# Optimization experiments

Hardware: AMD Instinct MI355X
Metric: run time of the kernel (lower is better)

The kernel has to match this reference:

```python
import jax, jax.numpy as jnp
import numpy as np

B, H, E, V = 128, 1024, 1024, 40000
L, S, A = 256, 10, 10
L_S, L_A = 1.0, 1.0  # s_copy_lambda / a_copy_lambda
NEG = -1e24


def setup_inputs():
    key = jax.random.key(0)
    ks = jax.random.split(key, 32)
    n = lambda i, shape: jax.random.normal(ks[i], shape, dtype=jnp.float32)
    p = lambda i, shape: jax.random.normal(ks[i], shape, dtype=jnp.float32) * 0.02
    rnn_in = 3 * E + H  # embed + history ctx (H) + state ctx (E) + action ctx (E)
    return {
        "inp": n(0, (B, 1, E)),
        "hidden": n(1, (1, B, H)),
        "hs_vectors": n(2, (B, L, H)),
        "state_gumbel_prob": jax.random.uniform(ks[3], (B, S, V), dtype=jnp.float32),
        "state_gumbel_embed": n(4, (B, S, E)),
        "action_gumbel_prob": jax.random.uniform(ks[5], (B, A, V), dtype=jnp.float32),
        "action_gumbel_embed": n(6, (B, A, E)),
        "history_lens": jax.random.randint(ks[7], (B,), 1, L + 1),
        "history_word_indices": jax.random.randint(ks[8], (B, L), 0, V),
        # history word mlp-attention
        "Wq_hist": p(9, (H, H)), "bq_hist": jnp.zeros((H,), jnp.float32),
        "Wm_hist": p(10, (H, H)), "v_hist": p(11, (H,)),
        # init_s_attn / init_a_attn (query H, memory E)
        "Wq_s": p(12, (H, H)), "bq_s": jnp.zeros((H,), jnp.float32),
        "Wm_s": p(13, (E, H)), "v_s": p(14, (H,)),
        "Wq_a": p(15, (H, H)), "bq_a": jnp.zeros((H,), jnp.float32),
        "Wm_a": p(16, (E, H)), "v_a": p(17, (H,)),
        # sparse_copy_attn (memory E+1)
        "Wq_sc": p(18, (H, H)), "bq_sc": jnp.zeros((H,), jnp.float32),
        "Wm_sc": p(19, (E + 1, H)), "v_sc": p(20, (H,)),
        # GRU (torch layout: [3H, in], gate order r,z,n)
        "W_ih": p(21, (3 * H, rnn_in)), "W_hh": p(22, (3 * H, H)),
        "b_ih": jnp.zeros((3 * H,), jnp.float32), "b_hh": jnp.zeros((3 * H,), jnp.float32),
        # output projection
        "W_out": p(23, (H, V)), "b_out": jnp.zeros((V,), jnp.float32),
    }


def _mlp_scores(q, mem, Wq, bq, Wm, v):
    # q: [B,1,H], mem: [B,L,M] -> additive-attention logits [B,1,L]
    t = jnp.tanh((q @ Wq + bq) + (mem @ Wm))  # [B,L,H]
    return (t @ v)[:, None, :]


def reference(inp, hidden, hs_vectors, state_gumbel_prob, state_gumbel_embed,
              action_gumbel_prob, action_gumbel_embed, history_lens,
              history_word_indices, Wq_hist, bq_hist, Wm_hist, v_hist,
              Wq_s, bq_s, Wm_s, v_s, Wq_a, bq_a, Wm_a, v_a,
              Wq_sc, bq_sc, Wm_sc, v_sc, W_ih, W_hh, b_ih, b_hh, W_out, b_out):
    q0 = jnp.transpose(hidden, (1, 0, 2))  # [B,1,H]
    # --- history word attention (masked mlp attention) ---
    hist_scores = _mlp_scores(q0, hs_vectors, Wq_hist, bq_hist, Wm_hist, v_hist)
    valid = jnp.arange(L)[None, None, :] < history_lens[:, None, None]
    hist_scores = jnp.where(valid, hist_scores, NEG)
    c_his = jax.nn.softmax(hist_scores, axis=-1) @ hs_vectors  # [B,1,H]
    # --- init_consult over state / action gumbel embeddings ---
    sw = jax.nn.softmax(_mlp_scores(q0, state_gumbel_embed, Wq_s, bq_s, Wm_s, v_s), axis=-1)
    c_state = sw @ state_gumbel_embed  # [B,1,E]
    aw = jax.nn.softmax(_mlp_scores(q0, action_gumbel_embed, Wq_a, bq_a, Wm_a, v_a), axis=-1)
    c_action = aw @ action_gumbel_embed  # [B,1,E]
    x = jnp.concatenate([inp, c_his, c_state, c_action], axis=-1)[:, 0, :]  # [B,3E+H]
    # --- single-step GRU cell (torch semantics, gate order r,z,n) ---
    h0 = hidden[0]
    gi = x @ W_ih.T + b_ih
    gh = h0 @ W_hh.T + b_hh
    ir, iz, inn = jnp.split(gi, 3, axis=-1)
    hr, hz, hn = jnp.split(gh, 3, axis=-1)
    r = jax.nn.sigmoid(ir + hr)
    z = jax.nn.sigmoid(iz + hz)
    nact = jnp.tanh(inn + r * hn)
    h_new = (1.0 - z) * nact + z * h0  # [B,H]
    # --- vocab logits + copy logits, joint softmax ---
    gene_logits = h_new @ W_out + b_out  # [B,V]
    cq = h_new[:, None, :]
    hs_logits = jnp.einsum('bqh,blh->bql', cq, hs_vectors)[:, 0, :]  # dot attn, [B,L]
    s_tag = jnp.zeros((B, S, 1), jnp.float32)
    a_tag = jnp.ones((B, A, 1), jnp.float32)
    st_logits = _mlp_scores(cq, jnp.concatenate([state_gumbel_embed, s_tag], -1), Wq_sc, bq_sc, Wm_sc, v_sc)[:, 0, :]
    ac_logits = _mlp_scores(cq, jnp.concatenate([action_gumbel_embed, a_tag], -1), Wq_sc, bq_sc, Wm_sc, v_sc)[:, 0, :]
    all_logits = jnp.concatenate([gene_logits, hs_logits, st_logits, ac_logits], axis=-1)
    wp = jax.nn.softmax(all_logits, axis=-1)  # [B, V+L+S+A]
    gene_p = wp[:, :V]
    hs_w = wp[:, V:V + L]
    st_w = wp[:, V + L:V + L + S]
    ac_w = wp[:, V + L + S:]
    # --- copy-distribution mixing ---
    scp = jnp.einsum('bs,bsv->bv', st_w, state_gumbel_prob)
    acp = jnp.einsum('ba,bav->bv', ac_w, action_gumbel_prob)
    gene_p = gene_p + L_S * scp + L_A * acp
    copy_p = jnp.zeros((B, V), jnp.float32).at[jnp.arange(B)[:, None], history_word_indices].add(hs_w)
    out = jnp.log(gene_p + copy_p)[:, None, :]  # [B,1,V]
    return out, h_new[None]
```

## Files before the change

### kernel.cpp

```cpp
#include <hip/hip_runtime.h>
#include <stdint.h>

typedef __attribute__((ext_vector_type(4))) float f32x4;
typedef __attribute__((ext_vector_type(2))) unsigned int u32x2;
typedef __attribute__((ext_vector_type(4))) unsigned int u32x4;
typedef __attribute__((ext_vector_type(8))) short bf16x8;

#define BV (128*40000)

__device__ __forceinline__ unsigned rne_bf16(float f) {
    unsigned x = __float_as_uint(f);
    return ((x + 0x7FFFu + ((x >> 16) & 1u)) >> 16) & 0xFFFFu;
}
__device__ __forceinline__ unsigned pack2(float a, float b) {
    return rne_bf16(a) | (rne_bf16(b) << 16);
}
__device__ __forceinline__ float bf2f(unsigned u) {
    return __uint_as_float((u & 0xFFFFu) << 16);
}
__device__ __forceinline__ float sigm(float x) { return 1.0f / (1.0f + expf(-x)); }
__device__ __forceinline__ float ftanh(float x) {
    float e = __expf(2.0f * x);
    return 1.0f - 2.0f / (e + 1.0f);
}

__device__ __forceinline__ void gload16(const void* g, void* l) {
    __builtin_amdgcn_global_load_lds(
        (const __attribute__((address_space(1))) unsigned*)g,
        (__attribute__((address_space(3))) unsigned*)l, 16, 0, 0);
}

struct BigArgs {
    const unsigned short *hs, *WmhT, *se, *ae, *WmsT, *WmaT;
    const int* lens;
    const float *qh_h, *bq_h, *v_h;
    const float *qh_s, *bq_s, *v_s;
    const float *qh_a, *bq_a, *v_a;
    float *hsc, *stsc, *acsc;
};

__global__ __launch_bounds__(512, 1) void k_big(BigArgs a) {
    __shared__ unsigned short As[2][16384];
    __shared__ unsigned short Bs[2][16384];

    int bid = blockIdx.x;
    int wg = (bid & 7) * 69 + (bid >> 3);

    const unsigned short *A, *Bt;
    const float *rb, *cb, *vv;
    float* out;
    int m0, n0, vrows, rpb;
    if (wg < 512) {
        int m = wg >> 2, n = wg & 3;
        A = a.hs; Bt = a.WmhT; rb = a.qh_h; cb = a.bq_h; vv = a.v_h; out = a.hsc;
        m0 = m << 8; n0 = n << 8; vrows = a.lens[m]; rpb = 256;
    } else {
        int r = wg - 512;
        int op = r / 20; r -= op * 20;
        int mt = r >> 2, nt = r & 3;
        if (op == 0) { A = a.se; Bt = a.WmsT; rb = a.qh_s; cb = a.bq_s; vv = a.v_s; out = a.stsc; }
        else         { A = a.ae; Bt = a.WmaT; rb = a.qh_a; cb = a.bq_a; vv = a.v_a; out = a.acsc; }
        m0 = mt << 8; n0 = nt << 8; vrows = 256; rpb = 10;
    }

    const int t = threadIdx.x, lane = t & 63, wv = t >> 6;
    const int l16 = lane & 15, lq = lane >> 4;
    const int wm = wv >> 2, wn = wv & 3;

    const int srowL = t >> 3;
    const int gccA = ((t & 7) ^ (srowL & 7)) << 3;
    const unsigned short* gA = A + (size_t)(m0 + srowL) * 1024 + gccA;
    const unsigned short* gB = Bt + (size_t)(n0 + srowL) * 1024 + gccA;

    f32x4 acc[8][4];
#pragma unroll
    for (int i = 0; i < 8; ++i)
#pragma unroll
        for (int j = 0; j < 4; ++j) acc[i][j] = (f32x4){0.f, 0.f, 0.f, 0.f};

    const int sw = l16 & 7;
    const int c0 = ((lq ^ sw) << 3);
    const int A0 = (wm << 13) + (l16 << 6);
    const int B0 = ((wn >> 1) << 13) + ((((wn & 1) << 6) + l16) << 6);

#define STAGE(kt, d)                                                          \
    {                                                                         \
        const unsigned short* ga_ = gA + (size_t)(kt) * 64;                   \
        const unsigned short* gb_ = gB + (size_t)(kt) * 64;                   \
        _Pragma("unroll")                                                     \
        for (int h_ = 0; h_ < 2; ++h_) {                                      \
            _Pragma("unroll")                                                 \
            for (int r_ = 0; r_ < 2; ++r_) {                                  \
                size_t go_ = (size_t)(h_ * 128 + r_ * 64) * 1024;             \
                int lo_ = h_ * 8192 + r_ * 4096 + (wv << 9);                  \
                gload16(ga_ + go_, &As[d][lo_]);                              \
                gload16(gb_ + go_, &Bs[d][lo_]);                              \
            }                                                                 \
        }                                                                     \
    }

    STAGE(0, 0);
    for (int kt = 0; kt < 16; ++kt) {
        int cur = kt & 1;
        if (kt < 15) {
            STAGE(kt + 1, cur ^ 1);
            asm volatile("s_waitcnt vmcnt(8)" ::: "memory");
        } else {
            asm volatile("s_waitcnt vmcnt(0)" ::: "memory");
        }
        __builtin_amdgcn_s_barrier();
        __builtin_amdgcn_sched_barrier(0);

        const unsigned short* ab = As[cur];
        const unsigned short* bb = Bs[cur];
        if (vrows > (wm << 7)) {
            bf16x8 bf[4][2];
#pragma unroll
            for (int nf = 0; nf < 4; ++nf) {
                bf[nf][0] = *(const bf16x8*)(bb + B0 + (nf << 10) + c0);
                bf[nf][1] = *(const bf16x8*)(bb + B0 + (nf << 10) + (c0 ^ 32));
            }
#pragma unroll
            for (int mf = 0; mf < 8; ++mf) {
                if ((wm << 7) + (mf << 4) < vrows) {
                    bf16x8 a0 = *(const bf16x8*)(ab + A0 + (mf << 10) + c0);
                    bf16x8 a1 = *(const bf16x8*)(ab + A0 + (mf << 10) + (c0 ^ 32));
#pragma unroll
                    for (int nf = 0; nf < 4; ++nf) {
                        acc[mf][nf] = __builtin_amdgcn_mfma_f32_16x16x32_bf16(a0, bf[nf][0], acc[mf][nf], 0, 0, 0);
                        acc[mf][nf] = __builtin_amdgcn_mfma_f32_16x16x32_bf16(a1, bf[nf][1], acc[mf][nf], 0, 0, 0);
                    }
                }
            }
        }
        __builtin_amdgcn_sched_barrier(0);
        __builtin_amdgcn_s_barrier();
    }
#undef STAGE

    float cbv[4], vvv[4];
    int gcs[4];
#pragma unroll
    for (int nf = 0; nf < 4; ++nf) {
        int gc = n0 + (wn << 6) + (nf << 4) + l16;
        gcs[nf] = gc; cbv[nf] = cb[gc]; vvv[nf] = vv[gc];
    }
#pragma unroll
    for (int mf = 0; mf < 8; ++mf) {
        int rloc = (wm << 7) + (mf << 4);
        if (rloc < vrows) {
#pragma unroll
            for (int r = 0; r < 4; ++r) {
                int gr = m0 + rloc + (lq << 2) + r;
                const float* rbp = rb + (size_t)(gr / rpb) * 1024;
                float s = 0.f;
#pragma unroll
                for (int nf = 0; nf < 4; ++nf) {
                    float x = acc[mf][nf][r] + rbp[gcs[nf]] + cbv[nf];
                    s += ftanh(x) * vvv[nf];
                }
#pragma unroll
                for (int m2 = 1; m2 < 16; m2 <<= 1) s += __shfl_xor(s, m2, 64);
                if (l16 == 0) atomicAdd(&out[gr], s);
            }
        }
    }
}

template<int EPI>
__device__ __forceinline__ void mgemm(
    const unsigned short* __restrict__ A, const unsigned short* __restrict__ Bt,
    float* __restrict__ out, const float* __restrict__ rb,
    const float* __restrict__ cb1, const float* __restrict__ cb2,
    const float* __restrict__ vvec,
    int m0, int n0, int kb, int ke, int ldk, int ldc, int rpb)
{
    __shared__ unsigned short As[2][4096];
    __shared__ unsigned short Bs[2][4096];
    const int t = threadIdx.x, lane = t & 63, wv = t >> 6;
    const int l16 = lane & 15, lq = lane >> 4;
    const int wm = wv >> 1, wn = wv & 1;

    const int srow = lane >> 2, scol = (lane & 3) << 3;
    const unsigned short* gA0 = A + (size_t)(m0 + (wv << 4) + srow) * ldk + kb + scol;
    const unsigned short* gA1 = gA0 + (size_t)64 * ldk;
    const unsigned short* gB0 = Bt + (size_t)(n0 + (wv << 4) + srow) * ldk + kb + scol;
    const unsigned short* gB1 = gB0 + (size_t)64 * ldk;
    unsigned short* lA0 = &As[0][wv << 9];
    unsigned short* lA1 = &As[0][(wv + 4) << 9];
    unsigned short* lB0 = &Bs[0][wv << 9];
    unsigned short* lB1 = &Bs[0][(wv + 4) << 9];

    f32x4 acc[4][4];
#pragma unroll
    for (int i = 0; i < 4; ++i)
#pragma unroll
        for (int j = 0; j < 4; ++j) acc[i][j] = (f32x4){0.f, 0.f, 0.f, 0.f};

    const int NS = (ke - kb) >> 5;
    gload16(gA0, lA0); gload16(gA1, lA1);
    gload16(gB0, lB0); gload16(gB1, lB1);

    for (int s = 0; s < NS; ++s) {
        __syncthreads();
        if (s + 1 < NS) {
            const int nb = (s + 1) & 1, ko = (s + 1) << 5;
            gload16(gA0 + ko, lA0 + (nb << 12)); gload16(gA1 + ko, lA1 + (nb << 12));
            gload16(gB0 + ko, lB0 + (nb << 12)); gload16(gB1 + ko, lB1 + (nb << 12));
        }
        const unsigned short* ab = As[s & 1];
        const unsigned short* bb = Bs[s & 1];
        bf16x8 af[4], bfv[4];
#pragma unroll
        for (int i = 0; i < 4; ++i)
            af[i] = *(const bf16x8*)(ab + (((wm << 6) + (i << 4) + l16) << 5) + (lq << 3));
#pragma unroll
        for (int i = 0; i < 4; ++i)
            bfv[i] = *(const bf16x8*)(bb + (((wn << 6) + (i << 4) + l16) << 5) + (lq << 3));
#pragma unroll
        for (int mf = 0; mf < 4; ++mf)
#pragma unroll
            for (int nf = 0; nf < 4; ++nf)
                acc[mf][nf] = __builtin_amdgcn_mfma_f32_16x16x32_bf16(af[mf], bfv[nf], acc[mf][nf], 0, 0, 0);
    }

    if (EPI == 1) {
#pragma unroll
        for (int mf = 0; mf < 4; ++mf) {
#pragma unroll
            for (int r = 0; r < 4; ++r) {
                int gr = m0 + (wm << 6) + (mf << 4) + (lq << 2) + r;
                const float* rbp = rb + (size_t)(gr / rpb) * 1024;
                float s = 0.0f;
#pragma unroll
                for (int nf = 0; nf < 4; ++nf) {
                    int gc = n0 + (wn << 6) + (nf << 4) + l16;
                    float xv = acc[mf][nf][r] + rbp[gc] + cb1[gc];
                    if (cb2) xv += cb2[gc];
                    s += ftanh(xv) * vvec[gc];
                }
#pragma unroll
                for (int msk = 1; msk < 16; msk <<= 1) s += __shfl_xor(s, msk, 64);
                if (l16 == 0) atomicAdd(&out[gr], s);
            }
        }
    } else {
#pragma unroll
        for (int mf = 0; mf < 4; ++mf) {
            int gr0 = m0 + (wm << 6) + (mf << 4) + (lq << 2);
#pragma unroll
            for (int nf = 0; nf < 4; ++nf) {
                int gc = n0 + (wn << 6) + (nf << 4) + l16;
#pragma unroll
                for (int r = 0; r < 4; ++r)
                    atomicAdd(&out[(size_t)(gr0 + r) * ldc + gc], acc[mf][nf][r]);
            }
        }
    }
}

__device__ __forceinline__ void gene_body(
    const unsigned short* __restrict__ hnb, const float* __restrict__ Wout,
    const float* __restrict__ b_out, float* __restrict__ out, int n0)
{
    __shared__ unsigned short As[2][4096];
    __shared__ unsigned short Bs[2][4096];
    const int t = threadIdx.x, lane = t & 63, wv = t >> 6;
    const int l16 = lane & 15, lq = lane >> 4;
    const int wm = wv >> 1, wn = wv & 1;

    const int srow = lane >> 2, scol = (lane & 3) << 3;
    const unsigned short* gA0 = hnb + (size_t)((wv << 4) + srow) * 1024 + scol;
    const unsigned short* gA1 = gA0 + (size_t)64 * 1024;
    unsigned short* lA0 = &As[0][wv << 9];
    unsigned short* lA1 = &As[0][(wv + 4) << 9];

    const int bn = t & 127, kh = t >> 7;
    const bool ok = (n0 + bn) < 40000;
    const float* gB = Wout + (size_t)(kh * 16) * 40000 + (n0 + bn);

    f32x4 acc[4][4];
#pragma unroll
    for (int i = 0; i < 4; ++i)
#pragma unroll
        for (int j = 0; j < 4; ++j) acc[i][j] = (f32x4){0.f, 0.f, 0.f, 0.f};

    auto stageB = [&](int buf, int ko) {
        const float* src = gB + (size_t)ko * 40000;
        float f[16];
#pragma unroll
        for (int j = 0; j < 16; ++j) f[j] = ok ? src[(size_t)j * 40000] : 0.0f;
        u32x4* d = (u32x4*)&Bs[buf][bn * 32 + kh * 16];
        d[0] = (u32x4){pack2(f[0],f[1]), pack2(f[2],f[3]), pack2(f[4],f[5]), pack2(f[6],f[7])};
        d[1] = (u32x4){pack2(f[8],f[9]), pack2(f[10],f[11]), pack2(f[12],f[13]), pack2(f[14],f[15])};
    };

    gload16(gA0, lA0); gload16(gA1, lA1); stageB(0, 0);
    for (int s = 0; s < 32; ++s) {
        __syncthreads();
        if (s + 1 < 32) {
            const int nb = (s + 1) & 1, ko = (s + 1) << 5;
            gload16(gA0 + ko, lA0 + (nb << 12)); gload16(gA1 + ko, lA1 + (nb << 12));
            stageB(nb, ko);
        }
        const unsigned short* ab = As[s & 1];
        const unsigned short* bb = Bs[s & 1];
        bf16x8 af[4], bfv[4];
#pragma unroll
        for (int i = 0; i < 4; ++i)
            af[i] = *(const bf16x8*)(ab + (((wm << 6) + (i << 4) + l16) << 5) + (lq << 3));
#pragma unroll
        for (int i = 0; i < 4; ++i)
            bfv[i] = *(const bf16x8*)(bb + (((wn << 6) + (i << 4) + l16) << 5) + (lq << 3));
#pragma unroll
        for (int mf = 0; mf < 4; ++mf)
#pragma unroll
            for (int nf = 0; nf < 4; ++nf)
                acc[mf][nf] = __builtin_amdgcn_mfma_f32_16x16x32_bf16(af[mf], bfv[nf], acc[mf][nf], 0, 0, 0);
    }
#pragma unroll
    for (int mf = 0; mf < 4; ++mf) {
        int gr0 = (wm << 6) + (mf << 4) + (lq << 2);
#pragma unroll
        for (int nf = 0; nf < 4; ++nf) {
            int gc = n0 + (wn << 6) + (nf << 4) + l16;
            if (gc < 40000) {
                float bo = b_out[gc];
#pragma unroll
                for (int r = 0; r < 4; ++r)
                    out[(size_t)(gr0 + r) * 40000 + gc] = acc[mf][nf][r] + bo;
            }
        }
    }
}

__global__ __launch_bounds__(256) void k_stac3(
    const unsigned short* se, const unsigned short* ae, const unsigned short* WmscT,
    const float* tagrow, const float* qsc, const float* bq_sc, const float* v_sc,
    float* stlg, float* aclg) {
    if (blockIdx.z == 0)
        mgemm<1>(se, WmscT, stlg, qsc, bq_sc, nullptr, v_sc, blockIdx.y * 128, blockIdx.x * 128, 0, 1024, 1024, 0, 10);
    else
        mgemm<1>(ae, WmscT, aclg, qsc, bq_sc, tagrow, v_sc, blockIdx.y * 128, blockIdx.x * 128, 0, 1024, 1024, 0, 10);
}

__global__ __launch_bounds__(256) void k_qh4(
    const unsigned short* q0, const unsigned short* W0, const unsigned short* W1,
    const unsigned short* W2, float* o0, float* o1, float* o2) {
    const unsigned short* W = W0; float* o = o0;
    if (blockIdx.z == 1) { W = W1; o = o1; }
    if (blockIdx.z == 2) { W = W2; o = o2; }
    int kb = blockIdx.y << 8;
    mgemm<2>(q0, W, o, nullptr, nullptr, nullptr, nullptr, 0, blockIdx.x * 128, kb, kb + 256, 1024, 1024, 1);
}

__global__ __launch_bounds__(256) void k_gigh2(
    const unsigned short* xb, const unsigned short* q0,
    const unsigned short* Wih, const unsigned short* Whh, float* gi, float* gh) {
    if (blockIdx.z == 0) {
        int kb = blockIdx.y << 9;
        mgemm<2>(xb, Wih, gi, nullptr, nullptr, nullptr, nullptr, 0, blockIdx.x * 128, kb, kb + 512, 4096, 3072, 1);
    } else {
        if (blockIdx.y >= 2) return;
        int kb = blockIdx.y << 9;
        mgemm<2>(q0, Whh, gh, nullptr, nullptr, nullptr, nullptr, 0, blockIdx.x * 128, kb, kb + 512, 1024, 3072, 1);
    }
}

__global__ __launch_bounds__(256) void k_qsc_gene(
    const unsigned short* hnb, const unsigned short* WqscT, float* qsc,
    const float* Wout, const float* b_out, float* out) {
    int id = blockIdx.x;
    if (id < 16) {
        int x = id & 7, kb = (id >> 3) << 9;
        mgemm<2>(hnb, WqscT, qsc, nullptr, nullptr, nullptr, nullptr, 0, x * 128, kb, kb + 512, 1024, 1024, 1);
    } else {
        gene_body(hnb, Wout, b_out, out, (id - 16) << 7);
    }
}

struct CvtArgs { const float* s[6]; unsigned short* d[6]; int pre[7]; };
__global__ __launch_bounds__(256) void k_cvt_all(CvtArgs a) {
    int total = a.pre[6];
    for (int i = blockIdx.x * 256 + threadIdx.x; i < total; i += gridDim.x * 256) {
        int seg = 0;
        while (i >= a.pre[seg + 1]) ++seg;
        int loc = i - a.pre[seg];
        const f32x4* s4 = (const f32x4*)a.s[seg] + (size_t)loc * 2;
        f32x4 q0 = s4[0], q1 = s4[1];
        ((u32x4*)a.d[seg])[loc] =
            (u32x4){pack2(q0[0],q0[1]), pack2(q0[2],q0[3]), pack2(q1[0],q1[1]), pack2(q1[2],q1[3])};
    }
}

struct TrArgs { const float* s[8]; unsigned short* d[8]; };
__global__ __launch_bounds__(256) void k_trcvt(TrArgs a) {
    __shared__ float tile[64][65];
    const float* in = a.s[blockIdx.z];
    unsigned short* ot = a.d[blockIdx.z];
    int k0 = blockIdx.y << 6, n0 = blockIdx.x << 6;
    int tr = threadIdx.x >> 6, tc = threadIdx.x & 63;
#pragma unroll
    for (int i = 0; i < 16; ++i) {
        int r = (i << 2) + tr;
        tile[r][tc] = in[(size_t)(k0 + r) * 1024 + n0 + tc];
    }
    __syncthreads();
#pragma unroll
    for (int i = 0; i < 16; ++i) {
        int r = (i << 2) + tr;
        ot[(size_t)(n0 + r) * 1024 + k0 + tc] = (unsigned short)rne_bf16(tile[tc][r]);
    }
}

__device__ __forceinline__ void softmax10(const float* src, float* dst) {
    float m = src[0];
    for (int i = 1; i < 10; ++i) m = fmaxf(m, src[i]);
    float z = 0.f, e[10];
    for (int i = 0; i < 10; ++i) { e[i] = expf(src[i] - m); z += e[i]; }
    float iz = 1.0f / z;
    for (int i = 0; i < 10; ++i) dst[i] = e[i] * iz;
}

__global__ __launch_bounds__(256) void k_ctx(
    const float* __restrict__ scores, const int* __restrict__ lens,
    const unsigned short* __restrict__ hs,
    const float* __restrict__ inp, const float* __restrict__ st_sc, const float* __restrict__ ac_sc,
    const unsigned short* __restrict__ se, const unsigned short* __restrict__ ae,
    unsigned short* __restrict__ xb) {
    int b = blockIdx.x, t = threadIdx.x;
    __shared__ float w[256];
    __shared__ float red[256];
    __shared__ float sw[10], aw[10];
    int len = lens[b];
    float s = scores[b * 256 + t];
    bool valid = t < len;
    red[t] = valid ? s : -3.0e38f;
    __syncthreads();
    for (int st = 128; st > 0; st >>= 1) { if (t < st) red[t] = fmaxf(red[t], red[t + st]); __syncthreads(); }
    float m = red[0];
    __syncthreads();
    float e = valid ? expf(s - m) : 0.0f;
    red[t] = e;
    __syncthreads();
    for (int st = 128; st > 0; st >>= 1) { if (t < st) red[t] += red[t + st]; __syncthreads(); }
    float Z = red[0];
    __syncthreads();
    w[t] = e / Z;
    if (t == 0) softmax10(st_sc + b * 10, sw);
    if (t == 64) softmax10(ac_sc + b * 10, aw);
    f32x4 iv = ((const f32x4*)(inp + (size_t)b * 1024))[t];
    *((u32x2*)(xb + (size_t)b * 4096) + t) = (u32x2){pack2(iv[0], iv[1]), pack2(iv[2], iv[3])};
    __syncthreads();
    float a0 = 0.f, a1 = 0.f, a2 = 0.f, a3 = 0.f;
    for (int l = 0; l < 256; ++l) {
        float wl = w[l];
        if (wl == 0.0f) continue;
        u32x2 u = *((const u32x2*)(hs + ((size_t)b * 256 + l) * 1024) + t);
        a0 += wl * bf2f(u[0]); a1 += wl * bf2f(u[0] >> 16);
        a2 += wl * bf2f(u[1]); a3 += wl * bf2f(u[1] >> 16);
    }
    *((u32x2*)(xb + (size_t)b * 4096 + 1024) + t) = (u32x2){pack2(a0, a1), pack2(a2, a3)};
    float cs0=0,cs1=0,cs2=0,cs3=0, ca0=0,ca1=0,ca2=0,ca3=0;
#pragma unroll
    for (int q = 0; q < 10; ++q) {
        u32x2 us = *((const u32x2*)(se + ((size_t)b * 10 + q) * 1024) + t);
        u32x2 ua = *((const u32x2*)(ae + ((size_t)b * 10 + q) * 1024) + t);
        float ws = sw[q], wa = aw[q];
        cs0 += ws * bf2f(us[0]); cs1 += ws * bf2f(us[0] >> 16);
        cs2 += ws * bf2f(us[1]); cs3 += ws * bf2f(us[1] >> 16);
        ca0 += wa * bf2f(ua[0]); ca1 += wa * bf2f(ua[0] >> 16);
        ca2 += wa * bf2f(ua[1]); ca3 += wa * bf2f(ua[1] >> 16);
    }
    *((u32x2*)(xb + (size_t)b * 4096 + 2048) + t) = (u32x2){pack2(cs0, cs1), pack2(cs2, cs3)};
    *((u32x2*)(xb + (size_t)b * 4096 + 3072) + t) = (u32x2){pack2(ca0, ca1), pack2(ca2, ca3)};
}

__global__ __launch_bounds__(1024) void k_gruhsl(
    const float* __restrict__ gi, const float* __restrict__ gh,
    const float* __restrict__ b_ih, const float* __restrict__ b_hh,
    const float* __restrict__ h0, float* __restrict__ hnew,
    unsigned short* __restrict__ hnb,
    const unsigned short* __restrict__ hs, float* __restrict__ hsl) {
    int b = blockIdx.x, j = threadIdx.x;
    size_t i = (size_t)b * 1024 + j;
    const float* gib = gi + (size_t)b * 3072;
    const float* ghb = gh + (size_t)b * 3072;
    float r = sigm(gib[j] + b_ih[j] + ghb[j] + b_hh[j]);
    float z = sigm(gib[1024 + j] + b_ih[1024 + j] + ghb[1024 + j] + b_hh[1024 + j]);
    float hn = ghb[2048 + j] + b_hh[2048 + j];
    float n = tanhf(gib[2048 + j] + b_ih[2048 + j] + r * hn);
    float h = (1.0f - z) * n + z * h0[i];
    hnew[i] = h;
    hnb[i] = (unsigned short)rne_bf16(h);
    __shared__ float hsm[1024];
    hsm[j] = h;
    __syncthreads();
    int wave = j >> 6, lane = j & 63;
    float hr[16];
#pragma unroll
    for (int k = 0; k < 16; ++k) hr[k] = hsm[lane * 16 + k];
    for (int l = wave; l < 256; l += 16) {
        const u32x4* row = (const u32x4*)(hs + ((size_t)b * 256 + l) * 1024);
        u32x4 u0 = row[lane * 2], u1 = row[lane * 2 + 1];
        float s = hr[0]*bf2f(u0[0]) + hr[1]*bf2f(u0[0]>>16) + hr[2]*bf2f(u0[1]) + hr[3]*bf2f(u0[1]>>16)
                + hr[4]*bf2f(u0[2]) + hr[5]*bf2f(u0[2]>>16) + hr[6]*bf2f(u0[3]) + hr[7]*bf2f(u0[3]>>16)
                + hr[8]*bf2f(u1[0]) + hr[9]*bf2f(u1[0]>>16) + hr[10]*bf2f(u1[1]) + hr[11]*bf2f(u1[1]>>16)
                + hr[12]*bf2f(u1[2]) + hr[13]*bf2f(u1[2]>>16) + hr[14]*bf2f(u1[3]) + hr[15]*bf2f(u1[3]>>16);
#pragma unroll
        for (int msk = 1; msk < 64; msk <<= 1) s += __shfl_xor(s, msk, 64);
        if (lane == 0) hsl[b * 256 + l] = s;
    }
}

__global__ __launch_bounds__(256) void k_smsc(
    const float* __restrict__ gene, const float* __restrict__ hsl,
    const float* __restrict__ stl, const float* __restrict__ acl,
    const int* __restrict__ hwi,
    float* __restrict__ mbuf, float* __restrict__ zbuf, float* __restrict__ copyp) {
    int b = blockIdx.x, t = threadIdx.x;
    __shared__ float red[256];
    const f32x4* g4 = (const f32x4*)(gene + (size_t)b * 40000);
    float mx = -3.0e38f;
    for (int i = t; i < 10000; i += 256) {
        f32x4 q = g4[i];
        mx = fmaxf(mx, fmaxf(fmaxf(q[0], q[1]), fmaxf(q[2], q[3])));
    }
    float hv = hsl[b * 256 + t];
    mx = fmaxf(mx, hv);
    if (t < 10) mx = fmaxf(mx, fmaxf(stl[b * 10 + t], acl[b * 10 + t]));
    red[t] = mx; __syncthreads();
    for (int s = 128; s > 0; s >>= 1) { if (t < s) red[t] = fmaxf(red[t], red[t + s]); __syncthreads(); }
    float m = red[0];
    __syncthreads();
    float sum = 0.f;
    for (int i = t; i < 10000; i += 256) {
        f32x4 q = g4[i];
        sum += expf(q[0]-m) + expf(q[1]-m) + expf(q[2]-m) + expf(q[3]-m);
    }
    sum += expf(hv - m);
    if (t < 10) sum += expf(stl[b * 10 + t] - m) + expf(acl[b * 10 + t] - m);
    red[t] = sum; __syncthreads();
    for (int s = 128; s > 0; s >>= 1) { if (t < s) red[t] += red[t + s]; __syncthreads(); }
    float Z = red[0];
    if (t == 0) { mbuf[b] = m; zbuf[b] = Z; }
    float wv = expf(hv - m) / Z;
    atomicAdd(copyp + (size_t)b * 40000 + hwi[b * 256 + t], wv);
}

__global__ __launch_bounds__(256) void k_final(
    float* __restrict__ gene_out, const float* __restrict__ copyp,
    const float* __restrict__ sprob, const float* __restrict__ aprob,
    const float* __restrict__ stl, const float* __restrict__ acl,
    const float* __restrict__ mbuf, const float* __restrict__ zbuf) {
    int b = blockIdx.y, t = threadIdx.x;
    __shared__ float sw[10], aw[10];
    float m = mbuf[b], iz = 1.0f / zbuf[b];
    if (t < 10) sw[t] = expf(stl[b * 10 + t] - m) * iz;
    if (t >= 64 && t < 74) aw[t - 64] = expf(acl[b * 10 + (t - 64)] - m) * iz;
    __syncthreads();
    int v4 = blockIdx.x * 256 + t;
    if (v4 < 10000) {
        size_t base = (size_t)b * 10000 + v4;
        f32x4 g = ((const f32x4*)gene_out)[base];
        f32x4 c = ((const f32x4*)copyp)[base];
        f32x4 acc;
#pragma unroll
        for (int j = 0; j < 4; ++j) acc[j] = expf(g[j] - m) * iz + c[j];
#pragma unroll
        for (int s = 0; s < 10; ++s) {
            f32x4 pv = ((const f32x4*)sprob)[((size_t)b * 10 + s) * 10000 + v4];
            f32x4 av = ((const f32x4*)aprob)[((size_t)b * 10 + s) * 10000 + v4];
            float ws = sw[s], wa = aw[s];
#pragma unroll
            for (int j = 0; j < 4; ++j) acc[j] += ws * pv[j] + wa * av[j];
        }
        f32x4 r;
#pragma unroll
        for (int j = 0; j < 4; ++j) r[j] = logf(acc[j]);
        ((f32x4*)gene_out)[base] = r;
    }
}

#define OFF_QH_H  0
#define OFF_QH_S  131072
#define OFF_QH_A  262144
#define OFF_QSC   393216
#define OFF_GI    524288
#define OFF_GH    917504
#define OFF_HSC   1310720
#define OFF_STSC  1343488
#define OFF_ACSC  1344768
#define OFF_STLG  1346048
#define OFF_ACLG  1347328
#define ZERO_FLOATS 1348608
#define OFF_HSL   1348608
#define OFF_M     1381376
#define OFF_Z     1381504
#define OFF_COPY  1381632
#define FLOAT_TOTAL 6501632
#define SO_HS     0
#define SO_SE     33554432
#define SO_AE     34865152
#define SO_Q0     36175872
#define SO_X      36306944
#define SO_HNB    36831232
#define SO_WQHT   36962304
#define SO_WQST   38010880
#define SO_WQAT   39059456
#define SO_WQSCT  40108032
#define SO_WMHT   41156608
#define SO_WMST   42205184
#define SO_WMAT   43253760
#define SO_WMSCT  44302336
#define SO_WIH    45350912
#define SO_WHH    57933824

extern "C" void kernel_launch(void* const* d_in, const int* in_sizes, int n_in,
                              void* d_out, int out_size, void* d_ws, size_t ws_size,
                              hipStream_t stream) {
    const float* inp     = (const float*)d_in[0];
    const float* hidden  = (const float*)d_in[1];
    const float* hs      = (const float*)d_in[2];
    const float* sprob   = (const float*)d_in[3];
    const float* se      = (const float*)d_in[4];
    const float* aprob   = (const float*)d_in[5];
    const float* ae      = (const float*)d_in[6];
    const int*   lens    = (const int*)d_in[7];
    const int*   hwi     = (const int*)d_in[8];
    const float* Wq_hist = (const float*)d_in[9];
    const float* bq_hist = (const float*)d_in[10];
    const float* Wm_hist = (const float*)d_in[11];
    const float* v_hist  = (const float*)d_in[12];
    const float* Wq_s    = (const float*)d_in[13];
    const float* bq_s    = (const float*)d_in[14];
    const float* Wm_s    = (const float*)d_in[15];
    const float* v_s     = (const float*)d_in[16];
    const float* Wq_a    = (const float*)d_in[17];
    const float* bq_a    = (const float*)d_in[18];
    const float* Wm_a    = (const float*)d_in[19];
    const float* v_a     = (const float*)d_in[20];
    const float* Wq_sc   = (const float*)d_in[21];
    const float* bq_sc   = (const float*)d_in[22];
    const float* Wm_sc   = (const float*)d_in[23];
    const float* v_sc    = (const float*)d_in[24];
    const float* W_ih    = (const float*)d_in[25];
    const float* W_hh    = (const float*)d_in[26];
    const float* b_ih    = (const float*)d_in[27];
    const float* b_hh    = (const float*)d_in[28];
    const float* W_out   = (const float*)d_in[29];
    const float* b_out   = (const float*)d_in[30];

    float* out  = (float*)d_out;
    float* w    = (float*)d_ws;
    float* hnew = out + BV;
    unsigned short* sb = (unsigned short*)(w + FLOAT_TOTAL);

    float* qh_h = w + OFF_QH_H;  float* qh_s = w + OFF_QH_S;  float* qh_a = w + OFF_QH_A;
    float* qsc  = w + OFF_QSC;   float* gi   = w + OFF_GI;    float* gh   = w + OFF_GH;
    float* hsc  = w + OFF_HSC;   float* stsc = w + OFF_STSC;  float* acsc = w + OFF_ACSC;
    float* stlg = w + OFF_STLG;  float* aclg = w + OFF_ACLG;
    float* hsl  = w + OFF_HSL;   float* mbuf = w + OFF_M;     float* zbuf = w + OFF_Z;
    float* copyp = w + OFF_COPY;

    unsigned short* hs_bf = sb + SO_HS;   unsigned short* se_bf = sb + SO_SE;
    unsigned short* ae_bf = sb + SO_AE;   unsigned short* q0_bf = sb + SO_Q0;
    unsigned short* x_bf  = sb + SO_X;    unsigned short* hnb   = sb + SO_HNB;
    unsigned short* WqhT  = sb + SO_WQHT; unsigned short* WqsT  = sb + SO_WQST;
    unsigned short* WqaT  = sb + SO_WQAT; unsigned short* WqscT = sb + SO_WQSCT;
    unsigned short* WmhT  = sb + SO_WMHT; unsigned short* WmsT  = sb + SO_WMST;
    unsigned short* WmaT  = sb + SO_WMAT; unsigned short* WmscT = sb + SO_WMSCT;
    unsigned short* WihB  = sb + SO_WIH;  unsigned short* WhhB  = sb + SO_WHH;

    dim3 blk(256);

    hipMemsetAsync(w, 0, (size_t)ZERO_FLOATS * 4, stream);
    hipMemsetAsync(copyp, 0, (size_t)BV * 4, stream);

    CvtArgs ca;
    ca.s[0]=hs; ca.s[1]=se; ca.s[2]=ae; ca.s[3]=hidden; ca.s[4]=W_ih; ca.s[5]=W_hh;
    ca.d[0]=hs_bf; ca.d[1]=se_bf; ca.d[2]=ae_bf; ca.d[3]=q0_bf; ca.d[4]=WihB; ca.d[5]=WhhB;
    ca.pre[0]=0; ca.pre[1]=4194304; ca.pre[2]=4358144; ca.pre[3]=4521984;
    ca.pre[4]=4538368; ca.pre[5]=6111232; ca.pre[6]=6504448;
    k_cvt_all<<<dim3(4096), blk, 0, stream>>>(ca);

    TrArgs ta;
    ta.s[0]=Wq_hist; ta.s[1]=Wq_s; ta.s[2]=Wq_a; ta.s[3]=Wq_sc;
    ta.s[4]=Wm_hist; ta.s[5]=Wm_s; ta.s[6]=Wm_a; ta.s[7]=Wm_sc;
    ta.d[0]=WqhT; ta.d[1]=WqsT; ta.d[2]=WqaT; ta.d[3]=WqscT;
    ta.d[4]=WmhT; ta.d[5]=WmsT; ta.d[6]=WmaT; ta.d[7]=WmscT;
    k_trcvt<<<dim3(16, 16, 8), blk, 0, stream>>>(ta);

    k_qh4<<<dim3(8, 4, 3), blk, 0, stream>>>(q0_bf, WqhT, WqsT, WqaT, qh_h, qh_s, qh_a);

    BigArgs ba;
    ba.hs = hs_bf; ba.WmhT = WmhT; ba.se = se_bf; ba.ae = ae_bf;
    ba.WmsT = WmsT; ba.WmaT = WmaT; ba.lens = lens;
    ba.qh_h = qh_h; ba.bq_h = bq_hist; ba.v_h = v_hist;
    ba.qh_s = qh_s; ba.bq_s = bq_s; ba.v_s = v_s;
    ba.qh_a = qh_a; ba.bq_a = bq_a; ba.v_a = v_a;
    ba.hsc = hsc; ba.stsc = stsc; ba.acsc = acsc;
    k_big<<<dim3(552), dim3(512), 0, stream>>>(ba);

    k_ctx<<<dim3(128), blk, 0, stream>>>(hsc, lens, hs_bf, inp, stsc, acsc, se_bf, ae_bf, x_bf);
    k_gigh2<<<dim3(24, 8, 2), blk, 0, stream>>>(x_bf, q0_bf, WihB, WhhB, gi, gh);
    k_gruhsl<<<dim3(128), dim3(1024), 0, stream>>>(gi, gh, b_ih, b_hh, hidden, hnew, hnb, hs_bf, hsl);
    k_qsc_gene<<<dim3(329), blk, 0, stream>>>(hnb, WqscT, qsc, W_out, b_out, out);
    k_stac3<<<dim3(8, 10, 2), blk, 0, stream>>>(se_bf, ae_bf, WmscT, Wm_sc + (size_t)1024 * 1024,
                                                qsc, bq_sc, v_sc, stlg, aclg);
    k_smsc<<<dim3(128), blk, 0, stream>>>(out, hsl, stlg, aclg, hwi, mbuf, zbuf, copyp);
    k_final<<<dim3(40, 128), blk, 0, stream>>>(out, copyp, sprob, aprob, stlg, aclg, mbuf, zbuf);

    (void)in_sizes; (void)n_in; (void)out_size; (void)ws_size;
}
```

Baseline: 575.4 us.

## Make k_big a persistent kernel with an atomic tile counter

Changes the big attention-score GEMM kernel from one workgroup per tile (552 blocks) to 256 persistent workgroups that take tiles from a global atomic counter. The small state/action tiles are scheduled first, followed by the history tiles, whose cost varies with history length. This targets the load imbalance caused by masked rows and the tail effect of a fixed grid. It adds a counter in the zeroed workspace, plus an atomic and two block barriers per tile. The MFMA issue order inside each k-step is also regrouped.

```diff
diff --git a/kernel.cpp b/kernel.cpp
--- a/kernel.cpp
+++ b/kernel.cpp
@@ -39,29 +39,10 @@
     float *hsc, *stsc, *acsc;
 };
 
-__global__ __launch_bounds__(512, 1) void k_big(BigArgs a) {
+__global__ __launch_bounds__(512, 1) void k_big(BigArgs a, int* __restrict__ ctr) {
     __shared__ unsigned short As[2][16384];
     __shared__ unsigned short Bs[2][16384];
-
-    int bid = blockIdx.x;
-    int wg = (bid & 7) * 69 + (bid >> 3);
-
-    const unsigned short *A, *Bt;
-    const float *rb, *cb, *vv;
-    float* out;
-    int m0, n0, vrows, rpb;
-    if (wg < 512) {
-        int m = wg >> 2, n = wg & 3;
-        A = a.hs; Bt = a.WmhT; rb = a.qh_h; cb = a.bq_h; vv = a.v_h; out = a.hsc;
-        m0 = m << 8; n0 = n << 8; vrows = a.lens[m]; rpb = 256;
-    } else {
-        int r = wg - 512;
-        int op = r / 20; r -= op * 20;
-        int mt = r >> 2, nt = r & 3;
-        if (op == 0) { A = a.se; Bt = a.WmsT; rb = a.qh_s; cb = a.bq_s; vv = a.v_s; out = a.stsc; }
-        else         { A = a.ae; Bt = a.WmaT; rb = a.qh_a; cb = a.bq_a; vv = a.v_a; out = a.acsc; }
-        m0 = mt << 8; n0 = nt << 8; vrows = 256; rpb = 10;
-    }
+    __shared__ int sTile;
 
     const int t = threadIdx.x, lane = t & 63, wv = t >> 6;
     const int l16 = lane & 15, lq = lane >> 4;
@@ -69,15 +50,6 @@
 
     const int srowL = t >> 3;
     const int gccA = ((t & 7) ^ (srowL & 7)) << 3;
-    const unsigned short* gA = A + (size_t)(m0 + srowL) * 1024 + gccA;
-    const unsigned short* gB = Bt + (size_t)(n0 + srowL) * 1024 + gccA;
-
-    f32x4 acc[8][4];
-#pragma unroll
-    for (int i = 0; i < 8; ++i)
-#pragma unroll
-        for (int j = 0; j < 4; ++j) acc[i][j] = (f32x4){0.f, 0.f, 0.f, 0.f};
-
     const int sw = l16 & 7;
     const int c0 = ((lq ^ sw) << 3);
     const int A0 = (wm << 13) + (l16 << 6);
@@ -99,72 +71,107 @@
         }                                                                     \
     }
 
-    STAGE(0, 0);
-    for (int kt = 0; kt < 16; ++kt) {
-        int cur = kt & 1;
-        if (kt < 15) {
-            STAGE(kt + 1, cur ^ 1);
-            asm volatile("s_waitcnt vmcnt(8)" ::: "memory");
+    for (;;) {
+        __syncthreads();
+        if (t == 0) sTile = atomicAdd(ctr, 1);
+        __syncthreads();
+        const int wg = sTile;
+        if (wg >= 552) return;
+
+        const unsigned short *A, *Bt;
+        const float *rb, *cb, *vv;
+        float* out;
+        int m0, n0, vrows, rpb;
+        if (wg < 40) {
+            int op = wg / 20, r = wg - op * 20;
+            int mt = r >> 2, nt = r & 3;
+            if (op == 0) { A = a.se; Bt = a.WmsT; rb = a.qh_s; cb = a.bq_s; vv = a.v_s; out = a.stsc; }
+            else         { A = a.ae; Bt = a.WmaT; rb = a.qh_a; cb = a.bq_a; vv = a.v_a; out = a.acsc; }
+            m0 = mt << 8; n0 = nt << 8; vrows = 256; rpb = 10;
         } else {
-            asm volatile("s_waitcnt vmcnt(0)" ::: "memory");
-        }
-        __builtin_amdgcn_s_barrier();
-        __builtin_amdgcn_sched_barrier(0);
-
-        const unsigned short* ab = As[cur];
-        const unsigned short* bb = Bs[cur];
-        if (vrows > (wm << 7)) {
-            bf16x8 bf[4][2];
-#pragma unroll
-            for (int nf = 0; nf < 4; ++nf) {
-                bf[nf][0] = *(const bf16x8*)(bb + B0 + (nf << 10) + c0);
-                bf[nf][1] = *(const bf16x8*)(bb + B0 + (nf << 10) + (c0 ^ 32));
+            int h = wg - 40;
+            int m = h >> 2, n = h & 3;
+            A = a.hs; Bt = a.WmhT; rb = a.qh_h; cb = a.bq_h; vv = a.v_h; out = a.hsc;
+            m0 = m << 8; n0 = n << 8; vrows = a.lens[m]; rpb = 256;
+        }
+
+        const unsigned short* gA = A + (size_t)(m0 + srowL) * 1024 + gccA;
+        const unsigned short* gB = Bt + (size_t)(n0 + srowL) * 1024 + gccA;
+
+        f32x4 acc[8][4];
+#pragma unroll
+        for (int i = 0; i < 8; ++i)
+#pragma unroll
+            for (int j = 0; j < 4; ++j) acc[i][j] = (f32x4){0.f, 0.f, 0.f, 0.f};
+
+        STAGE(0, 0);
+        for (int kt = 0; kt < 16; ++kt) {
+            int cur = kt & 1;
+            if (kt < 15) {
+                STAGE(kt + 1, cur ^ 1);
+                asm volatile("s_waitcnt vmcnt(8)" ::: "memory");
+            } else {
+                asm volatile("s_waitcnt vmcnt(0)" ::: "memory");
             }
-#pragma unroll
-            for (int mf = 0; mf < 8; ++mf) {
-                if ((wm << 7) + (mf << 4) < vrows) {
-                    bf16x8 a0 = *(const bf16x8*)(ab + A0 + (mf << 10) + c0);
-                    bf16x8 a1 = *(const bf16x8*)(ab + A0 + (mf << 10) + (c0 ^ 32));
-#pragma unroll
-                    for (int nf = 0; nf < 4; ++nf) {
-                        acc[mf][nf] = __builtin_amdgcn_mfma_f32_16x16x32_bf16(a0, bf[nf][0], acc[mf][nf], 0, 0, 0);
-                        acc[mf][nf] = __builtin_amdgcn_mfma_f32_16x16x32_bf16(a1, bf[nf][1], acc[mf][nf], 0, 0, 0);
+            __builtin_amdgcn_s_barrier();
+            __builtin_amdgcn_sched_barrier(0);
+
+            const unsigned short* ab = As[cur];
+            const unsigned short* bb = Bs[cur];
+            if (vrows > (wm << 7)) {
+                bf16x8 bf0[4], bf1[4];
+#pragma unroll
+                for (int nf = 0; nf < 4; ++nf) {
+                    bf0[nf] = *(const bf16x8*)(bb + B0 + (nf << 10) + c0);
+                    bf1[nf] = *(const bf16x8*)(bb + B0 + (nf << 10) + (c0 ^ 32));
+                }
+#pragma unroll
+                for (int mf = 0; mf < 8; ++mf) {
+                    if ((wm << 7) + (mf << 4) < vrows) {
+                        bf16x8 a0 = *(const bf16x8*)(ab + A0 + (mf << 10) + c0);
+                        bf16x8 a1 = *(const bf16x8*)(ab + A0 + (mf << 10) + (c0 ^ 32));
+#pragma unroll
+                        for (int nf = 0; nf < 4; ++nf)
+                            acc[mf][nf] = __builtin_amdgcn_mfma_f32_16x16x32_bf16(a0, bf0[nf], acc[mf][nf], 0, 0, 0);
+#pragma unroll
+                        for (int nf = 0; nf < 4; ++nf)
+                            acc[mf][nf] = __builtin_amdgcn_mfma_f32_16x16x32_bf16(a1, bf1[nf], acc[mf][nf], 0, 0, 0);
                     }
                 }
             }
-        }
-        __builtin_amdgcn_sched_barrier(0);
-        __builtin_amdgcn_s_barrier();
+            __builtin_amdgcn_sched_barrier(0);
+            __builtin_amdgcn_s_barrier();
+        }
+
+        float cbv[4], vvv[4];
+        int gcs[4];
+#pragma unroll
+        for (int nf = 0; nf < 4; ++nf) {
+            int gc = n0 + (wn << 6) + (nf << 4) + l16;
+            gcs[nf] = gc; cbv[nf] = cb[gc]; vvv[nf] = vv[gc];
+        }
+#pragma unroll
+        for (int mf = 0; mf < 8; ++mf) {
+            int rloc = (wm << 7) + (mf << 4);
+            if (rloc < vrows) {
+#pragma unroll
+                for (int r = 0; r < 4; ++r) {
+                    int gr = m0 + rloc + (lq << 2) + r;
+                    const float* rbp = rb + (size_t)(gr / rpb) * 1024;
+                    float s = 0.f;
+#pragma unroll
+                    for (int nf = 0; nf < 4; ++nf) {
+                        float x = acc[mf][nf][r] + rbp[gcs[nf]] + cbv[nf];
+                        s += ftanh(x) * vvv[nf];
+                    }
+#pragma unroll
+                    for (int m2 = 1; m2 < 16; m2 <<= 1) s += __shfl_xor(s, m2, 64);
+                    if (l16 == 0) atomicAdd(&out[gr], s);
+                }
+            }
+        }
     }
 #undef STAGE
-
-    float cbv[4], vvv[4];
-    int gcs[4];
-#pragma unroll
-    for (int nf = 0; nf < 4; ++nf) {
-        int gc = n0 + (wn << 6) + (nf << 4) + l16;
-        gcs[nf] = gc; cbv[nf] = cb[gc]; vvv[nf] = vv[gc];
-    }
-#pragma unroll
-    for (int mf = 0; mf < 8; ++mf) {
-        int rloc = (wm << 7) + (mf << 4);
-        if (rloc < vrows) {
-#pragma unroll
-            for (int r = 0; r < 4; ++r) {
-                int gr = m0 + rloc + (lq << 2) + r;
-                const float* rbp = rb + (size_t)(gr / rpb) * 1024;
-                float s = 0.f;
-#pragma unroll
-                for (int nf = 0; nf < 4; ++nf) {
-                    float x = acc[mf][nf][r] + rbp[gcs[nf]] + cbv[nf];
-                    s += ftanh(x) * vvv[nf];
-                }
-#pragma unroll
-                for (int m2 = 1; m2 < 16; m2 <<= 1) s += __shfl_xor(s, m2, 64);
-                if (l16 == 0) atomicAdd(&out[gr], s);
-            }
-        }
-    }
 }
 
 template<int EPI>
@@ -593,12 +600,13 @@
 #define OFF_ACSC  1344768
 #define OFF_STLG  1346048
 #define OFF_ACLG  1347328
-#define ZERO_FLOATS 1348608
-#define OFF_HSL   1348608
-#define OFF_M     1381376
-#define OFF_Z     1381504
-#define OFF_COPY  1381632
-#define FLOAT_TOTAL 6501632
+#define OFF_CTR   1348608
+#define ZERO_FLOATS 1348736
+#define OFF_HSL   1348736
+#define OFF_M     1381504
+#define OFF_Z     1381632
+#define OFF_COPY  1381760
+#define FLOAT_TOTAL 6501760
 #define SO_HS     0
 #define SO_SE     33554432
 #define SO_AE     34865152
@@ -662,6 +670,7 @@
     float* stlg = w + OFF_STLG;  float* aclg = w + OFF_ACLG;
     float* hsl  = w + OFF_HSL;   float* mbuf = w + OFF_M;     float* zbuf = w + OFF_Z;
     float* copyp = w + OFF_COPY;
+    int*   ctr  = (int*)(w + OFF_CTR);
 
     unsigned short* hs_bf = sb + SO_HS;   unsigned short* se_bf = sb + SO_SE;
     unsigned short* ae_bf = sb + SO_AE;   unsigned short* q0_bf = sb + SO_Q0;
@@ -700,7 +709,7 @@
     ba.qh_s = qh_s; ba.bq_s = bq_s; ba.v_s = v_s;
     ba.qh_a = qh_a; ba.bq_a = bq_a; ba.v_a = v_a;
     ba.hsc = hsc; ba.stsc = stsc; ba.acsc = acsc;
-    k_big<<<dim3(552), dim3(512), 0, stream>>>(ba);
+    k_big<<<dim3(256), dim3(512), 0, stream>>>(ba, ctr);
 
     k_ctx<<<dim3(128), blk, 0, stream>>>(hsc, lens, hs_bf, inp, stsc, acsc, se_bf, ae_bf, x_bf);
     k_gigh2<<<dim3(24, 8, 2), blk, 0, stream>>>(x_bf, q0_bf, WihB, WhhB, gi, gh);
```

Result: faster. 553.1 us (-3.9%).
